# Performance work log

Hardware: AMD Instinct MI355X
Metric: run time of the kernel (lower is better)

Reference implementation:

```python
import jax, jax.numpy as jnp
import numpy as np

EPS = 0.1  # eps added to covariance sums, as in torch cov()
N, D, N_CLASSES = 4096, 1024, 64


def setup_inputs() -> dict:
    key = jax.random.key(0)
    k1, k2 = jax.random.split(key)
    inputs = jax.random.normal(k1, (N, D), dtype=jnp.float32)
    targets = jax.random.randint(k2, (N,), 0, N_CLASSES, dtype=jnp.int32)
    return {"inputs": inputs, "targets": targets}


def _masked_sqdiff_sum(M, x):
    # Per-dim sum over masked pairs (i,j) of (x_i - x_j)^2, without
    # materializing the [n, n, d] difference tensor:
    #   sum_ij M_ij (x_id^2 + x_jd^2 - 2 x_id x_jd)
    row = M.sum(axis=1)  # [n]
    col = M.sum(axis=0)  # [n]
    x2 = x * x
    return row @ x2 + col @ x2 - 2.0 * jnp.sum(x * (M @ x), axis=0)  # [d]


def _jeffrey_loss(inputs, targets):
    n = inputs.shape[0]
    same = targets[:, None] == targets[None, :]
    eye = jnp.eye(n, dtype=bool)
    pos_m = (same & ~eye).astype(inputs.dtype)  # positive pairs, i != j
    neg_m = (~same).astype(inputs.dtype)        # negative pairs

    # Covariances are computed on detached diffs in the torch code
    xd = jax.lax.stop_gradient(inputs)
    cnt_pos = pos_m.sum()
    cnt_neg = neg_m.sum()
    sigma1 = (_masked_sqdiff_sum(pos_m, xd) + EPS) / cnt_pos  # [d]
    sigma0 = (_masked_sqdiff_sum(neg_m, xd) + EPS) / cnt_neg  # [d]
    weights = 1.0 / sigma0 - 1.0 / sigma1  # [d], constant w.r.t. grad

    # S[i, j] = sum_d weights_d * (x_i - x_j)_d^2, via gram expansion
    xw = inputs * weights            # [n, d]
    sq = jnp.sum(inputs * xw, axis=1)  # [n], sum_d w_d x_d^2
    S = sq[:, None] + sq[None, :] - 2.0 * inputs @ xw.T  # [n, n]

    # BCEWithLogitsLoss(mean): label 1 on positive pairs (logits a),
    # label 0 on negative pairs (logits b)
    loss_sum = jnp.sum(pos_m * jax.nn.softplus(-S)) + jnp.sum(neg_m * jax.nn.softplus(S))
    return loss_sum / (cnt_pos + cnt_neg)


def reference(inputs, targets):
    return _jeffrey_loss(inputs, targets)
```

## Files before the change

### kernel.cpp

```cpp
#include <hip/hip_runtime.h>
#include <stdint.h>

#define N_ROWS 4096
#define DIM    1024
#define NCLS   64
#define EPSV   0.1f

typedef __attribute__((ext_vector_type(4))) float f32x4;

__device__ __forceinline__ void async_cp16(const void* g, void* l) {
    __builtin_amdgcn_global_load_lds((const __attribute__((address_space(1))) void*)g,
                                     (__attribute__((address_space(3))) void*)l,
                                     16, 0, 0);
}

__device__ __forceinline__ float softplus(float x) {
    return fmaxf(x, 0.f) + __logf(1.f + __expf(-fabsf(x)));
}

__global__ __launch_bounds__(256) void k_cstats(const float* __restrict__ X,
                                                const int* __restrict__ tgt,
                                                float* __restrict__ csumR,
                                                float* __restrict__ csqR) {
    __shared__ int rows[N_ROWS];
    __shared__ int nrows_s;
    int tid = threadIdx.x;
    int c = blockIdx.x >> 2, q = blockIdx.x & 3;
    if (tid == 0) nrows_s = 0;
    __syncthreads();
    for (int i = tid; i < N_ROWS; i += 256)
        if (tgt[i] == c) { int p = atomicAdd(&nrows_s, 1); rows[p] = i; }
    __syncthreads();
    int n = nrows_s;
    int d = q * 256 + tid;
    float s = 0.f, qq = 0.f;
    #pragma unroll 4
    for (int r = 0; r < n; r++) {
        float x = X[(size_t)rows[r] * DIM + d];
        s += x; qq += x * x;
    }
    csumR[c * DIM + d] = s;
    csqR [c * DIM + d] = qq;
}

__global__ __launch_bounds__(128) void k_weights(const int* __restrict__ tgt,
                                                 const float* __restrict__ csumR,
                                                 const float* __restrict__ csqR,
                                                 float* __restrict__ w,
                                                 float* __restrict__ scal,
                                                 float* __restrict__ loss_out) {
    __shared__ int hist[NCLS];
    __shared__ float redw[2];
    int tid = threadIdx.x, b = blockIdx.x;
    if (tid < NCLS) hist[tid] = 0;
    __syncthreads();
    for (int i = tid; i < N_ROWS; i += 128) atomicAdd(&hist[tgt[i]], 1);
    __syncthreads();
    long long sp = 0, ss = 0;
    for (int c = 0; c < NCLS; c++) { long long cc = hist[c]; sp += cc * (cc - 1); ss += cc * cc; }
    float cnt_pos = (float)sp;
    float cnt_neg = (float)((long long)N_ROWS * N_ROWS - ss);
    int d = b * 128 + tid;
    float A = 0.f, X2 = 0.f, T = 0.f, SS = 0.f;
    #pragma unroll 8
    for (int c = 0; c < NCLS; c++) {
        float s = csumR[c * DIM + d];
        float q = csqR [c * DIM + d];
        A += (float)hist[c] * q; X2 += q; T += s; SS += s * s;
    }
    float posnum = 2.f * (A - SS);
    float negnum = 2.f * ((float)N_ROWS * X2 - A - T * T + SS);
    float wd = cnt_neg / (negnum + EPSV) - cnt_pos / (posnum + EPSV);
    w[d] = wd;
    float m = wd * wd;
    for (int off = 32; off; off >>= 1) m += __shfl_down(m, off, 64);
    int wv = tid >> 6, ln = tid & 63;
    if (ln == 0) redw[wv] = m;
    __syncthreads();
    if (b == 0 && tid == 0) {
        float ms = (redw[0] + redw[1]) / 128.f;
        scal[0] = exp2f(roundf(log2f(sqrtf(ms) + 1e-30f)));
        loss_out[0] = 0.0f;
    }
}

__global__ __launch_bounds__(256) void k_prep(const float* __restrict__ X,
                                              const float* __restrict__ w,
                                              const float* __restrict__ scal,
                                              unsigned int* __restrict__ Xb8,
                                              unsigned int* __restrict__ XWb8,
                                              float* __restrict__ sq) {
    int row = blockIdx.x, tid = threadIdx.x;
    float inv_sw = 1.0f / scal[0];
    float4 x  = ((const float4*)(X + (size_t)row * DIM))[tid];
    float4 ww = ((const float4*)w)[tid];
    float4 xw = make_float4(x.x * ww.x, x.y * ww.y, x.z * ww.z, x.w * ww.w);
    float p = x.x * xw.x + x.y * xw.y + x.z * xw.z + x.w * xw.w;
    unsigned ux = __builtin_amdgcn_cvt_pk_fp8_f32(x.x, x.y, 0, false);
    ux = __builtin_amdgcn_cvt_pk_fp8_f32(x.z, x.w, ux, true);
    unsigned uw = __builtin_amdgcn_cvt_pk_fp8_f32(xw.x * inv_sw, xw.y * inv_sw, 0, false);
    uw = __builtin_amdgcn_cvt_pk_fp8_f32(xw.z * inv_sw, xw.w * inv_sw, uw, true);
    int t = tid >> 3, q = (tid >> 1) & 3, o = tid & 1;
    int s = (row >> 2) & 3;
    int widx = row * 256 + t * 8 + (q ^ s) * 2 + o;
    Xb8 [widx] = ux;
    XWb8[widx] = uw;
    for (int off = 32; off; off >>= 1) p += __shfl_down(p, off, 64);
    __shared__ float red[4];
    int wv = tid >> 6, ln = tid & 63;
    if (ln == 0) red[wv] = p;
    __syncthreads();
    if (tid == 0) sq[row] = red[0] + red[1] + red[2] + red[3];
}

__global__ __launch_bounds__(256) void k_gemm_loss(const unsigned char* __restrict__ Xb8,
                                                   const unsigned char* __restrict__ XWb8,
                                                   const float* __restrict__ sq,
                                                   const int* __restrict__ tgt,
                                                   const float* __restrict__ scal,
                                                   float* __restrict__ loss) {
    __shared__ __align__(16) unsigned char As[4][128 * 32];
    __shared__ __align__(16) unsigned char Bs[4][128 * 32];
    __shared__ float sqI[128], sqJ[128];
    __shared__ int   tIs[128], tJs[128];
    __shared__ float red[4];

    int tid = threadIdx.x;
    int wave = tid >> 6, lane = tid & 63;

    int g = blockIdx.x & 7, s = blockIdx.x >> 3;
    int j0 = g, j1 = 15 - g, j2 = 16 + g, j3 = 31 - g;
    int n0 = j0 + 1, n1 = j1 + 1, n2 = j2 + 1;
    int jt, it;
    if      (s < n0)           { jt = j0; it = s; }
    else if (s < n0 + n1)      { jt = j1; it = s - n0; }
    else if (s < n0 + n1 + n2) { jt = j2; it = s - n0 - n1; }
    else                       { jt = j3; it = s - n0 - n1 - n2; }

    bool isA = wave < 2;
    const unsigned char* srcb = (isA ? Xb8 : XWb8) + (size_t)((isA ? it : jt) * 128) * DIM;
    unsigned char* slab = isA ? &As[0][0] : &Bs[0][0];
    const unsigned char* gp[2];
    unsigned char* lb[2];
    #pragma unroll
    for (int si = 0; si < 2; si++) {
        int ch = (wave & 1) * 128 + si * 64 + lane;
        int r = ch >> 1, h = ch & 1;
        gp[si] = srcb + (size_t)r * DIM + h * 16;
        lb[si] = slab + ((wave & 1) * 128 + si * 64) * 16;
    }

    int lr = lane & 15, kq = lane >> 4;
    int offA[4], offB[4];
    int wrow = (wave >> 1) * 64, wcol = (wave & 1) * 64;
    #pragma unroll
    for (int mi = 0; mi < 4; mi++) {
        int row = wrow + mi * 16 + lr;
        offA[mi] = row * 32 + (kq ^ ((row >> 2) & 3)) * 8;
        int col = wcol + mi * 16 + lr;
        offB[mi] = col * 32 + (kq ^ ((col >> 2) & 3)) * 8;
    }

    f32x4 acc[4][4];
    #pragma unroll
    for (int i = 0; i < 4; i++)
        #pragma unroll
        for (int j = 0; j < 4; j++) acc[i][j] = (f32x4){0.f, 0.f, 0.f, 0.f};

    #pragma unroll
    for (int st = 0; st < 3; st++)
        #pragma unroll
        for (int si = 0; si < 2; si++)
            async_cp16(gp[si] + st * 32, lb[si] + st * 4096);

    for (int kk = 0; kk < 32; kk++) {
        if      (kk < 30)  asm volatile("s_waitcnt vmcnt(4)" ::: "memory");
        else if (kk == 30) asm volatile("s_waitcnt vmcnt(2)" ::: "memory");
        else               asm volatile("s_waitcnt vmcnt(0)" ::: "memory");
        asm volatile("s_barrier" ::: "memory");
        if (kk < 29) {
            #pragma unroll
            for (int si = 0; si < 2; si++)
                async_cp16(gp[si] + (kk + 3) * 32, lb[si] + ((kk + 3) & 3) * 4096);
        }
        int rd = kk & 3;
        const unsigned char* Ab = As[rd];
        const unsigned char* Bb = Bs[rd];
        long long av[4], bv[4];
        #pragma unroll
        for (int i = 0; i < 4; i++) {
            av[i] = *(const long long*)(Ab + offA[i]);
            bv[i] = *(const long long*)(Bb + offB[i]);
        }
        #pragma unroll
        for (int i = 0; i < 4; i++)
            #pragma unroll
            for (int j = 0; j < 4; j++)
                acc[i][j] = __builtin_amdgcn_mfma_f32_16x16x32_fp8_fp8(av[i], bv[j], acc[i][j], 0, 0, 0);
    }

    __syncthreads();
    if (tid < 128) { sqI[tid] = sq[it * 128 + tid]; tIs[tid] = tgt[it * 128 + tid]; }
    else { int u = tid - 128; sqJ[u] = sq[jt * 128 + u]; tJs[u] = tgt[jt * 128 + u]; }
    __syncthreads();

    float sw2 = 2.0f * scal[0];
    float sum = 0.f;
    bool diagTile = (it == jt);
    #pragma unroll
    for (int j = 0; j < 4; j++) {
        int col = wcol + j * 16 + (lane & 15);
        float sj = sqJ[col]; int tj = tJs[col];
        #pragma unroll
        for (int i = 0; i < 4; i++) {
            int rbase = wrow + i * 16 + (lane >> 4) * 4;
            #pragma unroll
            for (int r = 0; r < 4; r++) {
                int rowp = rbase + r;
                float S = sqI[rowp] + sj - sw2 * acc[i][j][r];
                float v;
                if (tIs[rowp] == tj) v = (diagTile && rowp == col) ? 0.f : softplus(-S);
                else                 v = softplus(S);
                sum += v;
            }
        }
    }
    float scale = (diagTile ? 1.f : 2.f) * (1.f / ((float)N_ROWS * (float)(N_ROWS - 1)));
    sum *= scale;
    for (int off = 32; off; off >>= 1) sum += __shfl_down(sum, off, 64);
    if (lane == 0) red[wave] = sum;
    __syncthreads();
    if (tid == 0) atomicAdd(loss, red[0] + red[1] + red[2] + red[3]);
}

extern "C" void kernel_launch(void* const* d_in, const int* in_sizes, int n_in,
                              void* d_out, int out_size, void* d_ws, size_t ws_size,
                              hipStream_t stream) {
    const float* X  = (const float*)d_in[0];
    const int* tgt  = (const int*)d_in[1];
    float* out = (float*)d_out;
    char* ws = (char*)d_ws;
    const size_t MB = 1u << 20;

    float* w      = (float*)ws;
    float* sq     = (float*)(ws + 4096);
    float* scal   = (float*)(ws + 24576);
    unsigned int* Xb8  = (unsigned int*)(ws + 1 * MB);
    unsigned int* XWb8 = (unsigned int*)(ws + 5 * MB);
    float* csumR  = (float*)(ws + 9 * MB);
    float* csqR   = (float*)(ws + 9 * MB + 256 * 1024);

    k_cstats  <<<256,  256, 0, stream>>>(X, tgt, csumR, csqR);
    k_weights <<<8,    128, 0, stream>>>(tgt, csumR, csqR, w, scal, out);
    k_prep    <<<4096, 256, 0, stream>>>(X, w, scal, Xb8, XWb8, sq);
    k_gemm_loss<<<528, 256, 0, stream>>>((const unsigned char*)Xb8, (const unsigned char*)XWb8,
                                         sq, tgt, scal, out);
}
```

Baseline: 128.8 us.

## Fuse four kernels into one persistent kernel with grid-wide barriers

```diff
diff --git a/kernel.cpp b/kernel.cpp
--- a/kernel.cpp
+++ b/kernel.cpp
@@ -5,6 +5,7 @@
 #define DIM    1024
 #define NCLS   64
 #define EPSV   0.1f
+#define GRID   528
 
 typedef __attribute__((ext_vector_type(4))) float f32x4;
 
@@ -18,127 +19,133 @@
     return fmaxf(x, 0.f) + __logf(1.f + __expf(-fabsf(x)));
 }
 
-__global__ __launch_bounds__(256) void k_cstats(const float* __restrict__ X,
-                                                const int* __restrict__ tgt,
-                                                float* __restrict__ csumR,
-                                                float* __restrict__ csqR) {
-    __shared__ int rows[N_ROWS];
-    __shared__ int nrows_s;
-    int tid = threadIdx.x;
-    int c = blockIdx.x >> 2, q = blockIdx.x & 3;
-    if (tid == 0) nrows_s = 0;
-    __syncthreads();
-    for (int i = tid; i < N_ROWS; i += 256)
-        if (tgt[i] == c) { int p = atomicAdd(&nrows_s, 1); rows[p] = i; }
-    __syncthreads();
-    int n = nrows_s;
-    int d = q * 256 + tid;
-    float s = 0.f, qq = 0.f;
-    #pragma unroll 4
-    for (int r = 0; r < n; r++) {
-        float x = X[(size_t)rows[r] * DIM + d];
-        s += x; qq += x * x;
-    }
-    csumR[c * DIM + d] = s;
-    csqR [c * DIM + d] = qq;
-}
-
-__global__ __launch_bounds__(128) void k_weights(const int* __restrict__ tgt,
-                                                 const float* __restrict__ csumR,
-                                                 const float* __restrict__ csqR,
-                                                 float* __restrict__ w,
-                                                 float* __restrict__ scal,
-                                                 float* __restrict__ loss_out) {
-    __shared__ int hist[NCLS];
-    __shared__ float redw[2];
-    int tid = threadIdx.x, b = blockIdx.x;
-    if (tid < NCLS) hist[tid] = 0;
-    __syncthreads();
-    for (int i = tid; i < N_ROWS; i += 128) atomicAdd(&hist[tgt[i]], 1);
-    __syncthreads();
-    long long sp = 0, ss = 0;
-    for (int c = 0; c < NCLS; c++) { long long cc = hist[c]; sp += cc * (cc - 1); ss += cc * cc; }
-    float cnt_pos = (float)sp;
-    float cnt_neg = (float)((long long)N_ROWS * N_ROWS - ss);
-    int d = b * 128 + tid;
-    float A = 0.f, X2 = 0.f, T = 0.f, SS = 0.f;
-    #pragma unroll 8
-    for (int c = 0; c < NCLS; c++) {
-        float s = csumR[c * DIM + d];
-        float q = csqR [c * DIM + d];
-        A += (float)hist[c] * q; X2 += q; T += s; SS += s * s;
-    }
-    float posnum = 2.f * (A - SS);
-    float negnum = 2.f * ((float)N_ROWS * X2 - A - T * T + SS);
-    float wd = cnt_neg / (negnum + EPSV) - cnt_pos / (posnum + EPSV);
-    w[d] = wd;
-    float m = wd * wd;
-    for (int off = 32; off; off >>= 1) m += __shfl_down(m, off, 64);
-    int wv = tid >> 6, ln = tid & 63;
-    if (ln == 0) redw[wv] = m;
-    __syncthreads();
-    if (b == 0 && tid == 0) {
-        float ms = (redw[0] + redw[1]) / 128.f;
-        scal[0] = exp2f(roundf(log2f(sqrtf(ms) + 1e-30f)));
-        loss_out[0] = 0.0f;
-    }
-}
-
-__global__ __launch_bounds__(256) void k_prep(const float* __restrict__ X,
-                                              const float* __restrict__ w,
-                                              const float* __restrict__ scal,
-                                              unsigned int* __restrict__ Xb8,
-                                              unsigned int* __restrict__ XWb8,
-                                              float* __restrict__ sq) {
-    int row = blockIdx.x, tid = threadIdx.x;
-    float inv_sw = 1.0f / scal[0];
-    float4 x  = ((const float4*)(X + (size_t)row * DIM))[tid];
-    float4 ww = ((const float4*)w)[tid];
-    float4 xw = make_float4(x.x * ww.x, x.y * ww.y, x.z * ww.z, x.w * ww.w);
-    float p = x.x * xw.x + x.y * xw.y + x.z * xw.z + x.w * xw.w;
-    unsigned ux = __builtin_amdgcn_cvt_pk_fp8_f32(x.x, x.y, 0, false);
-    ux = __builtin_amdgcn_cvt_pk_fp8_f32(x.z, x.w, ux, true);
-    unsigned uw = __builtin_amdgcn_cvt_pk_fp8_f32(xw.x * inv_sw, xw.y * inv_sw, 0, false);
-    uw = __builtin_amdgcn_cvt_pk_fp8_f32(xw.z * inv_sw, xw.w * inv_sw, uw, true);
-    int t = tid >> 3, q = (tid >> 1) & 3, o = tid & 1;
-    int s = (row >> 2) & 3;
-    int widx = row * 256 + t * 8 + (q ^ s) * 2 + o;
-    Xb8 [widx] = ux;
-    XWb8[widx] = uw;
-    for (int off = 32; off; off >>= 1) p += __shfl_down(p, off, 64);
-    __shared__ float red[4];
-    int wv = tid >> 6, ln = tid & 63;
-    if (ln == 0) red[wv] = p;
-    __syncthreads();
-    if (tid == 0) sq[row] = red[0] + red[1] + red[2] + red[3];
-}
-
-__global__ __launch_bounds__(256) void k_gemm_loss(const unsigned char* __restrict__ Xb8,
-                                                   const unsigned char* __restrict__ XWb8,
-                                                   const float* __restrict__ sq,
-                                                   const int* __restrict__ tgt,
-                                                   const float* __restrict__ scal,
-                                                   float* __restrict__ loss) {
-    __shared__ __align__(16) unsigned char As[4][128 * 32];
-    __shared__ __align__(16) unsigned char Bs[4][128 * 32];
+__device__ __forceinline__ void gbar(unsigned int* cnt, unsigned int target) {
+    __syncthreads();
+    if (threadIdx.x == 0) {
+        __threadfence();
+        atomicAdd(cnt, 1u);
+        while (__hip_atomic_load(cnt, __ATOMIC_RELAXED, __HIP_MEMORY_SCOPE_AGENT) < target)
+            __builtin_amdgcn_s_sleep(8);
+        __threadfence();
+    }
+    __syncthreads();
+}
+
+__global__ __launch_bounds__(256, 3) void k_fused(
+        const float* __restrict__ X, const int* __restrict__ tgt,
+        float* __restrict__ w, float* __restrict__ scal,
+        float* __restrict__ sq,
+        unsigned int* __restrict__ Xb8, unsigned int* __restrict__ XWb8,
+        float* __restrict__ csumR, float* __restrict__ csqR,
+        unsigned int* __restrict__ syncc, float* __restrict__ out) {
+    __shared__ __align__(16) unsigned char As[4][4096];
+    __shared__ __align__(16) unsigned char Bs[4][4096];
     __shared__ float sqI[128], sqJ[128];
     __shared__ int   tIs[128], tJs[128];
     __shared__ float red[4];
-
-    int tid = threadIdx.x;
+    __shared__ int   hist[NCLS];
+    __shared__ int   nrows_s;
+
+    int tid = threadIdx.x, blk = blockIdx.x;
     int wave = tid >> 6, lane = tid & 63;
 
-    int g = blockIdx.x & 7, s = blockIdx.x >> 3;
-    int j0 = g, j1 = 15 - g, j2 = 16 + g, j3 = 31 - g;
+    if (blk < 256) {
+        int* rows = (int*)&As[0][0];
+        int c = blk >> 2, q = blk & 3;
+        if (tid == 0) nrows_s = 0;
+        __syncthreads();
+        for (int i = tid; i < N_ROWS; i += 256)
+            if (tgt[i] == c) { int p = atomicAdd(&nrows_s, 1); rows[p] = i; }
+        __syncthreads();
+        int n = nrows_s;
+        int d = q * 256 + tid;
+        float s = 0.f, qq = 0.f;
+        #pragma unroll 4
+        for (int r = 0; r < n; r++) {
+            float x = X[(size_t)rows[r] * DIM + d];
+            s += x; qq += x * x;
+        }
+        csumR[c * DIM + d] = s;
+        csqR [c * DIM + d] = qq;
+    }
+    gbar(syncc, GRID);
+
+    if (blk < 4) {
+        if (tid < NCLS) hist[tid] = 0;
+        __syncthreads();
+        for (int i = tid; i < N_ROWS; i += 256) atomicAdd(&hist[tgt[i]], 1);
+        __syncthreads();
+        long long sp = 0, ss = 0;
+        for (int c = 0; c < NCLS; c++) { long long cc = hist[c]; sp += cc * (cc - 1); ss += cc * cc; }
+        float cnt_pos = (float)sp;
+        float cnt_neg = (float)((long long)N_ROWS * N_ROWS - ss);
+        int d = blk * 256 + tid;
+        float A = 0.f, X2 = 0.f, T = 0.f, SS = 0.f;
+        #pragma unroll 8
+        for (int c = 0; c < NCLS; c++) {
+            float s = csumR[c * DIM + d];
+            float q = csqR [c * DIM + d];
+            A += (float)hist[c] * q; X2 += q; T += s; SS += s * s;
+        }
+        float posnum = 2.f * (A - SS);
+        float negnum = 2.f * ((float)N_ROWS * X2 - A - T * T + SS);
+        float wd = cnt_neg / (negnum + EPSV) - cnt_pos / (posnum + EPSV);
+        w[d] = wd;
+        if (blk == 0) {
+            float m = wd * wd;
+            for (int off = 32; off; off >>= 1) m += __shfl_down(m, off, 64);
+            if ((tid & 63) == 0) red[wave] = m;
+            __syncthreads();
+            if (tid == 0) {
+                float ms = (red[0] + red[1] + red[2] + red[3]) / 256.f;
+                scal[0] = exp2f(roundf(log2f(sqrtf(ms) + 1e-30f)));
+                out[0] = 0.0f;
+            }
+        }
+    }
+    gbar(syncc, 2 * GRID);
+
+    {
+        float inv_sw = 1.0f / scal[0];
+        #pragma unroll 1
+        for (int i = 0; i < 8; i++) {
+            int row = blk + i * GRID;
+            bool act = row < N_ROWS;
+            float4 x = act ? ((const float4*)(X + (size_t)row * DIM))[tid]
+                           : make_float4(0.f, 0.f, 0.f, 0.f);
+            float4 ww = ((const float4*)w)[tid];
+            float4 xw = make_float4(x.x * ww.x, x.y * ww.y, x.z * ww.z, x.w * ww.w);
+            float p = x.x * xw.x + x.y * xw.y + x.z * xw.z + x.w * xw.w;
+            unsigned ux = __builtin_amdgcn_cvt_pk_fp8_f32(x.x, x.y, 0, false);
+            ux = __builtin_amdgcn_cvt_pk_fp8_f32(x.z, x.w, ux, true);
+            unsigned uw = __builtin_amdgcn_cvt_pk_fp8_f32(xw.x * inv_sw, xw.y * inv_sw, 0, false);
+            uw = __builtin_amdgcn_cvt_pk_fp8_f32(xw.z * inv_sw, xw.w * inv_sw, uw, true);
+            int t = tid >> 3, q = (tid >> 1) & 3, o = tid & 1;
+            int ssw = (row >> 2) & 3;
+            int widx = row * 256 + t * 8 + (q ^ ssw) * 2 + o;
+            if (act) { Xb8[widx] = ux; XWb8[widx] = uw; }
+            for (int off = 32; off; off >>= 1) p += __shfl_down(p, off, 64);
+            if ((tid & 63) == 0) red[wave] = p;
+            __syncthreads();
+            if (act && tid == 0) sq[row] = red[0] + red[1] + red[2] + red[3];
+            __syncthreads();
+        }
+    }
+    gbar(syncc, 3 * GRID);
+
+    int g = blk & 7, s = blk >> 3;
+    int j0 = g, j1 = 15 - g, j2 = 16 + g;
     int n0 = j0 + 1, n1 = j1 + 1, n2 = j2 + 1;
     int jt, it;
     if      (s < n0)           { jt = j0; it = s; }
     else if (s < n0 + n1)      { jt = j1; it = s - n0; }
     else if (s < n0 + n1 + n2) { jt = j2; it = s - n0 - n1; }
-    else                       { jt = j3; it = s - n0 - n1 - n2; }
-
+    else                       { jt = 31 - g; it = s - n0 - n1 - n2; }
+
+    const unsigned char* Xc  = (const unsigned char*)Xb8;
+    const unsigned char* XWc = (const unsigned char*)XWb8;
     bool isA = wave < 2;
-    const unsigned char* srcb = (isA ? Xb8 : XWb8) + (size_t)((isA ? it : jt) * 128) * DIM;
+    const unsigned char* srcb = (isA ? Xc : XWc) + (size_t)((isA ? it : jt) * 128) * DIM;
     unsigned char* slab = isA ? &As[0][0] : &Bs[0][0];
     const unsigned char* gp[2];
     unsigned char* lb[2];
@@ -230,7 +237,7 @@
     for (int off = 32; off; off >>= 1) sum += __shfl_down(sum, off, 64);
     if (lane == 0) red[wave] = sum;
     __syncthreads();
-    if (tid == 0) atomicAdd(loss, red[0] + red[1] + red[2] + red[3]);
+    if (tid == 0) atomicAdd(out, red[0] + red[1] + red[2] + red[3]);
 }
 
 extern "C" void kernel_launch(void* const* d_in, const int* in_sizes, int n_in,
@@ -245,14 +252,13 @@
     float* w      = (float*)ws;
     float* sq     = (float*)(ws + 4096);
     float* scal   = (float*)(ws + 24576);
-    unsigned int* Xb8  = (unsigned int*)(ws + 1 * MB);
-    unsigned int* XWb8 = (unsigned int*)(ws + 5 * MB);
+    unsigned int* syncc = (unsigned int*)(ws + 32768);
+    unsigned int* Xb8   = (unsigned int*)(ws + 1 * MB);
+    unsigned int* XWb8  = (unsigned int*)(ws + 5 * MB);
     float* csumR  = (float*)(ws + 9 * MB);
     float* csqR   = (float*)(ws + 9 * MB + 256 * 1024);
 
-    k_cstats  <<<256,  256, 0, stream>>>(X, tgt, csumR, csqR);
-    k_weights <<<8,    128, 0, stream>>>(tgt, csumR, csqR, w, scal, out);
-    k_prep    <<<4096, 256, 0, stream>>>(X, w, scal, Xb8, XWb8, sq);
-    k_gemm_loss<<<528, 256, 0, stream>>>((const unsigned char*)Xb8, (const unsigned char*)XWb8,
-                                         sq, tgt, scal, out);
-}
+    hipMemsetAsync(syncc, 0, 64, stream);
+    k_fused<<<GRID, 256, 0, stream>>>(X, tgt, w, scal, sq, Xb8, XWb8,
+                                      csumR, csqR, syncc, out);
+}
```

After: 247.2 us. 1.92x slower.
